# Performance work log

Hardware: AMD Instinct MI355X
Metric: run time of the kernel (lower is better)

The kernel has to match this reference:

```python
import jax, jax.numpy as jnp
import numpy as np
import math

# ---- static config (matches init_kwargs) ----
N_USERS = 40000
N_ITEMS = 30000
N_ENTITIES = 80000
N_REL = 8            # edge_type in [1, N_REL), relation_emb has N_REL-1 rows
DIM = 64
N_HEADS = 2
D_K = DIM // N_HEADS
N_HOPS = 2
E_KG = 800000
E_UI = 600000


def setup_inputs() -> dict:
    key = jax.random.key(0)
    ks = jax.random.split(key, 10)
    return {
        "user_emb": jax.random.normal(ks[0], (N_USERS, DIM), jnp.float32) * 0.1,
        "entity_emb": jax.random.normal(ks[1], (N_ENTITIES, DIM), jnp.float32) * 0.1,
        "relation_emb": jax.random.normal(ks[2], (N_REL - 1, DIM), jnp.float32) * 0.1,
        "W_Q": jax.random.normal(ks[3], (DIM, DIM), jnp.float32) * (1.0 / math.sqrt(DIM)),
        "inter_edge_w": jax.random.uniform(ks[4], (E_UI,), jnp.float32),
        "edge_head": jax.random.randint(ks[5], (E_KG,), 0, N_ENTITIES, jnp.int32),
        "edge_tail": jax.random.randint(ks[6], (E_KG,), 0, N_ENTITIES, jnp.int32),
        "edge_type": jax.random.randint(ks[7], (E_KG,), 1, N_REL, jnp.int32),
        "inter_user": jax.random.randint(ks[8], (E_UI,), 0, N_USERS, jnp.int32),
        "inter_item": jax.random.randint(ks[9], (E_UI,), 0, N_ENTITIES, jnp.int32),
    }


def _seg_softmax(x, seg, n):
    """Numerically-stable softmax over edges grouped by segment id (scatter_softmax)."""
    m = jax.ops.segment_max(x, seg, num_segments=n)
    m = jnp.where(jnp.isneginf(m), 0.0, m)          # empty segments
    ex = jnp.exp(x - m[seg])
    s = jax.ops.segment_sum(ex, seg, num_segments=n)
    return ex / (s[seg] + 1e-16)


def _edge_attn(entity_emb, relation_emb, W_Q, head, tail, etype):
    """Per-edge multi-head attention logits: q_h . (k_h * rel_h) / sqrt(d_k). [E, H]"""
    q = (entity_emb[head] @ W_Q).reshape(-1, N_HEADS, D_K)
    k = (entity_emb[tail] @ W_Q).reshape(-1, N_HEADS, D_K)
    k = k * relation_emb[etype - 1].reshape(-1, N_HEADS, D_K)
    return (q * k).sum(-1) * (1.0 / math.sqrt(D_K))


def _l2norm(x):
    return x / jnp.maximum(jnp.linalg.norm(x, axis=-1, keepdims=True), 1e-12)


def reference(user_emb, entity_emb, relation_emb, W_Q, inter_edge_w,
              edge_head, edge_tail, edge_type, inter_user, inter_item):
    # ---- norm_attn_computer (logits detached in original torch code) ----
    logits = jax.lax.stop_gradient(
        _edge_attn(entity_emb, relation_emb, W_Q, edge_head, edge_tail, edge_type).mean(-1))  # [E]
    score = _seg_softmax(logits, edge_head, N_ENTITIES)
    deg = jax.ops.segment_sum(jnp.ones((E_KG,), jnp.float32), edge_head, num_segments=N_ENTITIES)
    edge_attn_score = score * deg[edge_head]                                   # [E]
    item_attn_sumed = (jax.ops.segment_sum(logits, edge_head, num_segments=N_ENTITIES)
                       + jax.ops.segment_sum(logits, edge_tail, num_segments=N_ENTITIES))[:N_ITEMS]

    # ---- HGT message passing hops (mess_dropout=False) ----
    e, u = entity_emb, user_emb
    e_res, u_res = entity_emb, user_emb
    for _ in range(N_HOPS):
        attn = _edge_attn(e, relation_emb, W_Q, edge_head, edge_tail, edge_type)  # [E, H]
        s = _seg_softmax(attn, edge_head, N_ENTITIES)                              # [E, H]
        neigh = (e[edge_tail] * relation_emb[edge_type - 1]).reshape(-1, N_HEADS, D_K) * s[..., None]
        e_agg = jax.ops.segment_sum(neigh.reshape(-1, DIM), edge_head, num_segments=N_ENTITIES)
        # bipartite user<->item aggregation with interaction weights
        u_agg = jax.ops.segment_sum(inter_edge_w[:, None] * e[inter_item], inter_user,
                                    num_segments=N_USERS)
        e_agg = e_agg + jax.ops.segment_sum(inter_edge_w[:, None] * u[inter_user], inter_item,
                                            num_segments=N_ENTITIES)
        e, u = _l2norm(e_agg), _l2norm(u_agg)
        e_res, u_res = e_res + e, u_res + u

    node_res_emb = jnp.concatenate([u_res, e_res], axis=0)   # [N_USERS+N_ENTITIES, DIM]
    return node_res_emb, edge_attn_score, item_attn_sumed
```

## Files before the change

### kernel.cpp

```cpp
#include <hip/hip_runtime.h>
#include <math.h>

#define NUSERS 40000
#define NENT   80000
#define NITEMS 30000
#define DIM    64
#define EKG    800000
#define EUI    600000
#define NTOT   (NENT + NUSERS + NENT)
#define UBASE  NENT
#define IBASE  (NENT + NUSERS)

struct __align__(8) us4 { unsigned short x, y, z, w; };
static __device__ __forceinline__ float b2f(unsigned short b) {
    return __uint_as_float(((unsigned)b) << 16);
}
static __device__ __forceinline__ unsigned short f2b(float f) {
    unsigned u = __float_as_uint(f);
    return (unsigned short)((u + 0x7FFFu + ((u >> 16) & 1u)) >> 16);
}
static __device__ __forceinline__ float4 ld4b(const unsigned short* p) {
    us4 v = *(const us4*)p;
    return make_float4(b2f(v.x), b2f(v.y), b2f(v.z), b2f(v.w));
}
static __device__ __forceinline__ void st4b(unsigned short* p, float a, float b, float c, float d) {
    us4 v = {f2b(a), f2b(b), f2b(c), f2b(d)};
    *(us4*)p = v;
}

static __device__ __forceinline__ float grp16_sum(float v) {
    v += __shfl_xor(v, 1);
    v += __shfl_xor(v, 2);
    v += __shfl_xor(v, 4);
    v += __shfl_xor(v, 8);
    return v;
}

__global__ void count_kernel(const int* __restrict__ ehead, const int* __restrict__ etail,
                             const int* __restrict__ etype,
                             const int* __restrict__ iuser, const int* __restrict__ iitem,
                             int* __restrict__ cnt,
                             int* __restrict__ hrK, int* __restrict__ hrU, int* __restrict__ hrI,
                             int* __restrict__ tpack) {
    int e = blockIdx.x * blockDim.x + threadIdx.x;
    if (e < EKG) {
        int h = __builtin_nontemporal_load(&ehead[e]);
        int r = atomicAdd(&cnt[h], 1);
        hrK[e] = (h << 15) | r;
        tpack[e] = __builtin_nontemporal_load(&etail[e]) |
                   ((__builtin_nontemporal_load(&etype[e]) - 1) << 20);
    }
    if (e < EUI) {
        int u = __builtin_nontemporal_load(&iuser[e]);
        int r = atomicAdd(&cnt[UBASE + u], 1);
        hrU[e] = (u << 16) | r;
        int it = __builtin_nontemporal_load(&iitem[e]);
        int r2 = atomicAdd(&cnt[IBASE + it], 1);
        hrI[e] = (it << 15) | r2;
    }
}

#define SCHUNK 2048
#define SBLOCKS ((NTOT + SCHUNK - 1) / SCHUNK)

__global__ void scanA_kernel(const int* __restrict__ cnt, int* __restrict__ bsum) {
    int b = blockIdx.x, tid = threadIdx.x;
    int base = b * SCHUNK + tid * 8;
    int ts = 0;
#pragma unroll
    for (int k = 0; k < 8; k++) {
        int i = base + k;
        ts += (i < NTOT) ? cnt[i] : 0;
    }
#pragma unroll
    for (int d = 1; d < 64; d <<= 1) ts += __shfl_xor(ts, d);
    __shared__ int ws[4];
    if ((tid & 63) == 0) ws[tid >> 6] = ts;
    __syncthreads();
    if (tid == 0) bsum[b] = ws[0] + ws[1] + ws[2] + ws[3];
}

__global__ void scanB_kernel(const int* __restrict__ bsum, int* __restrict__ bpre,
                             int* __restrict__ off) {
    int lane = threadIdx.x;
    int carry = 0;
    for (int base = 0; base < SBLOCKS; base += 64) {
        int i = base + lane;
        int x = (i < SBLOCKS) ? bsum[i] : 0;
        int inc = x;
#pragma unroll
        for (int d = 1; d < 64; d <<= 1) {
            int t = __shfl_up(inc, d);
            if (lane >= d) inc += t;
        }
        if (i < SBLOCKS) bpre[i] = carry + inc - x;
        carry += __shfl(inc, 63);
    }
    if (lane == 0) off[NTOT] = carry;
}

__global__ void scanC_kernel(const int* __restrict__ cnt, const int* __restrict__ bpre,
                             int* __restrict__ off) {
    __shared__ int wtot[4];
    int b = blockIdx.x, tid = threadIdx.x, lane = tid & 63, wid = tid >> 6;
    int base = b * SCHUNK + tid * 8;
    int vals[8];
    int ts = 0;
#pragma unroll
    for (int k = 0; k < 8; k++) {
        int i = base + k;
        int x = (i < NTOT) ? cnt[i] : 0;
        vals[k] = ts;
        ts += x;
    }
    int inc = ts;
#pragma unroll
    for (int d = 1; d < 64; d <<= 1) {
        int t = __shfl_up(inc, d);
        if (lane >= d) inc += t;
    }
    if (lane == 63) wtot[wid] = inc;
    __syncthreads();
    int wbase = 0;
    for (int w = 0; w < wid; w++) wbase += wtot[w];
    int tbase = bpre[b] + wbase + (inc - ts);
#pragma unroll
    for (int k = 0; k < 8; k++) {
        int i = base + k;
        if (i < NTOT) off[i] = tbase + vals[k];
    }
}

__global__ void fillKG_kernel(const int* __restrict__ hrK, const int* __restrict__ tpack,
                              const int* __restrict__ off,
                              int* __restrict__ tt, int* __restrict__ eid, int lo, int hi) {
    int e = blockIdx.x * blockDim.x + threadIdx.x;
    if (e >= EKG) return;
    int v = __builtin_nontemporal_load(&hrK[e]);
    int h = ((unsigned)v) >> 15;
    if (h < (unsigned)lo || h >= (unsigned)hi) return;
    int p = off[h] + (v & 0x7FFF);
    tt[p] = __builtin_nontemporal_load(&tpack[e]);
    eid[p] = e;
}

__global__ void fillUIu_kernel(const int* __restrict__ hrU, const int* __restrict__ iitem,
                               const float* __restrict__ iwin, const int* __restrict__ off,
                               int2* __restrict__ upack, int lo, int hi) {
    int e = blockIdx.x * blockDim.x + threadIdx.x;
    if (e >= EUI) return;
    int v = __builtin_nontemporal_load(&hrU[e]);
    int u = ((unsigned)v) >> 16;
    if (u < (unsigned)lo || u >= (unsigned)hi) return;
    int p = off[UBASE + u] - EKG + (v & 0xFFFF);
    upack[p] = make_int2(__builtin_nontemporal_load(&iitem[e]),
                         __float_as_int(__builtin_nontemporal_load(&iwin[e])));
}

__global__ void fillUIi_kernel(const int* __restrict__ hrI, const int* __restrict__ iuser,
                               const float* __restrict__ iwin, const int* __restrict__ off,
                               int2* __restrict__ ipack, int lo, int hi) {
    int e = blockIdx.x * blockDim.x + threadIdx.x;
    if (e >= EUI) return;
    int v = __builtin_nontemporal_load(&hrI[e]);
    int it = ((unsigned)v) >> 15;
    if (it < (unsigned)lo || it >= (unsigned)hi) return;
    int p = off[IBASE + it] - (EKG + EUI) + (v & 0x7FFF);
    ipack[p] = make_int2(__builtin_nontemporal_load(&iuser[e]),
                         __float_as_int(__builtin_nontemporal_load(&iwin[e])));
}

__global__ void cvt_kernel(const float* __restrict__ in, unsigned short* __restrict__ out,
                           int n4) {
    int i = blockIdx.x * blockDim.x + threadIdx.x;
    if (i >= n4) return;
    float4 v = *(const float4*)(in + (size_t)i * 4);
    st4b(out + (size_t)i * 4, v.x, v.y, v.z, v.w);
}

template <int MODE>
__global__ void gemm_wq_kernel(const float* __restrict__ Xf,
                               const unsigned short* __restrict__ Xb_in,
                               const float* __restrict__ W,
                               unsigned short* __restrict__ Pb,
                               unsigned short* __restrict__ Xb_out) {
    __shared__ float Wl[64 * 64];
    int tid = threadIdx.x;
    for (int i = tid; i < 64 * 64; i += 256) Wl[i] = W[i];
    __syncthreads();
    int rloc = tid >> 4;
    int c4 = (tid & 15) * 4;
    int row = blockIdx.x * 16 + rloc;
    float ax = 0, ay = 0, az = 0, aw = 0;
#pragma unroll 8
    for (int d = 0; d < 64; d++) {
        float xv = (MODE == 0) ? Xf[(size_t)row * DIM + d] : b2f(Xb_in[(size_t)row * DIM + d]);
        const float4 w = *(const float4*)&Wl[d * 64 + c4];
        ax += xv * w.x;
        ay += xv * w.y;
        az += xv * w.z;
        aw += xv * w.w;
    }
    st4b(Pb + (size_t)row * DIM + c4, ax, ay, az, aw);
    if (MODE == 0) {
        const float4 xx = *(const float4*)(Xf + (size_t)row * DIM + c4);
        st4b(Xb_out + (size_t)row * DIM + c4, xx.x, xx.y, xx.z, xx.w);
    }
}

template <bool HOP0>
__global__ void hop_kernel(const unsigned short* __restrict__ Pb,
                           const unsigned short* __restrict__ eb,
                           const unsigned short* __restrict__ ub,
                           const float* __restrict__ rel,
                           const int* __restrict__ off,
                           const int* __restrict__ tt, const int* __restrict__ eid,
                           const int2* __restrict__ upack, const int2* __restrict__ ipack,
                           const float* __restrict__ ebase, const float* __restrict__ ubase,
                           const unsigned short* __restrict__ eprevb,
                           const unsigned short* __restrict__ uprevb,
                           float* __restrict__ e_res, float* __restrict__ u_res,
                           unsigned short* __restrict__ enxtb, unsigned short* __restrict__ unxtb,
                           float* __restrict__ logit, float* __restrict__ edge_score,
                           float* __restrict__ item_sum) {
    __shared__ float srel[7 * DIM];
    int tid = threadIdx.x;
    for (int i = tid; i < 7 * DIM; i += 256) srel[i] = rel[i];
    __syncthreads();
    int g = tid >> 4, l = tid & 15;
    int v = blockIdx.x * 16 + g;
    const float sc = 0.17677669529663687f;
    float ax = 0, ay = 0, az = 0, aw = 0;

    if (v < NENT) {
        int o0 = off[v], o1 = off[v + 1];
        int deg = o1 - o0;
        const float4 q = ld4b(Pb + (size_t)v * DIM + l * 4);
        float s_h = 0.f;
        float s_lm = 0.f, lsum = 0.f;
        for (int j = o0; j < o1; j++) {
            unsigned t = (unsigned)tt[j];
            int tail = t & 0xFFFFF;
            int r = t >> 20;
            const float4 k = ld4b(Pb + (size_t)tail * DIM + l * 4);
            const float4 ev = ld4b(eb + (size_t)tail * DIM + l * 4);
            const float4 rv = *(const float4*)(srel + r * DIM + l * 4);
            float part = q.x * k.x * rv.x + q.y * k.y * rv.y + q.z * k.z * rv.z + q.w * k.w * rv.w;
            part += __shfl_xor(part, 1);
            part += __shfl_xor(part, 2);
            part += __shfl_xor(part, 4);
            part *= sc;
            float w = __expf(part);
            s_h += w;
            ax += w * ev.x * rv.x;
            ay += w * ev.y * rv.y;
            az += w * ev.z * rv.z;
            aw += w * ev.w * rv.w;
            if (HOP0) {
                float other = __shfl_xor(part, 8);
                float lm = 0.5f * (part + other);
                s_lm += __expf(lm);
                lsum += lm;
                if (l == 0) {
                    logit[j] = lm;
                    if (tail < NITEMS) atomicAdd(&item_sum[tail], lm);
                }
            }
        }
        float inv_sh = 1.0f / (s_h + 1e-16f);
        ax *= inv_sh;
        ay *= inv_sh;
        az *= inv_sh;
        aw *= inv_sh;
        if (HOP0) {
            if (l == 0 && v < NITEMS && deg > 0) atomicAdd(&item_sum[v], lsum);
            float inv_slm = 1.0f / (s_lm + 1e-16f);
            float degf = (float)deg;
            for (int j = o0 + l; j < o1; j += 16) {
                edge_score[eid[j]] = __expf(logit[j]) * inv_slm * degf;
            }
        }
        int p0 = off[IBASE + v] - (EKG + EUI);
        int p1 = off[IBASE + v + 1] - (EKG + EUI);
        for (int j = p0; j < p1; j++) {
            int2 up = ipack[j];
            float w = __int_as_float(up.y);
            const float4 uv = ld4b(ub + (size_t)up.x * DIM + l * 4);
            ax += w * uv.x;
            ay += w * uv.y;
            az += w * uv.z;
            aw += w * uv.w;
        }
        float nsq = grp16_sum(ax * ax + ay * ay + az * az + aw * aw);
        float invn = 1.0f / fmaxf(sqrtf(nsq), 1e-12f);
        float ox = ax * invn, oy = ay * invn, oz = az * invn, ow = aw * invn;
        size_t base = (size_t)v * DIM + l * 4;
        if (HOP0) {
            st4b(enxtb + base, ox, oy, oz, ow);
        } else {
            const float4 b0 = *(const float4*)(ebase + base);
            const float4 p0v = ld4b(eprevb + base);
            float4 ro = {b0.x + p0v.x + ox, b0.y + p0v.y + oy, b0.z + p0v.z + oz,
                         b0.w + p0v.w + ow};
            *(float4*)(e_res + base) = ro;
        }
    } else {
        int u = v - NENT;
        int p0 = off[UBASE + u] - EKG;
        int p1 = off[UBASE + u + 1] - EKG;
        for (int j = p0; j < p1; j++) {
            int2 up = upack[j];
            float w = __int_as_float(up.y);
            const float4 ev = ld4b(eb + (size_t)up.x * DIM + l * 4);
            ax += w * ev.x;
            ay += w * ev.y;
            az += w * ev.z;
            aw += w * ev.w;
        }
        float nsq = grp16_sum(ax * ax + ay * ay + az * az + aw * aw);
        float invn = 1.0f / fmaxf(sqrtf(nsq), 1e-12f);
        float ox = ax * invn, oy = ay * invn, oz = az * invn, ow = aw * invn;
        size_t base = (size_t)u * DIM + l * 4;
        if (HOP0) {
            st4b(unxtb + base, ox, oy, oz, ow);
        } else {
            const float4 b0 = *(const float4*)(ubase + base);
            const float4 p0v = ld4b(uprevb + base);
            float4 ro = {b0.x + p0v.x + ox, b0.y + p0v.y + oy, b0.z + p0v.z + oz,
                         b0.w + p0v.w + ow};
            *(float4*)(u_res + base) = ro;
        }
    }
}

extern "C" void kernel_launch(void* const* d_in, const int* in_sizes, int n_in,
                              void* d_out, int out_size, void* d_ws, size_t ws_size,
                              hipStream_t stream) {
    const float* user_emb   = (const float*)d_in[0];
    const float* entity_emb = (const float*)d_in[1];
    const float* rel        = (const float*)d_in[2];
    const float* W_Q        = (const float*)d_in[3];
    const float* iwin       = (const float*)d_in[4];
    const int* ehead        = (const int*)d_in[5];
    const int* etail        = (const int*)d_in[6];
    const int* etype        = (const int*)d_in[7];
    const int* iuser        = (const int*)d_in[8];
    const int* iitem        = (const int*)d_in[9];

    float* out        = (float*)d_out;
    float* u_res      = out;
    float* e_res      = out + (size_t)NUSERS * DIM;
    float* edge_score = out + (size_t)(NUSERS + NENT) * DIM;
    float* item_sum   = edge_score + EKG;

    char* w = (char*)d_ws;
    auto alloc = [&](size_t bytes) -> void* {
        void* p = (void*)w;
        w += (bytes + 255) & ~(size_t)255;
        return p;
    };
    unsigned short* Pb  = (unsigned short*)alloc((size_t)NENT * DIM * 2);
    unsigned short* e0b = (unsigned short*)alloc((size_t)NENT * DIM * 2);
    unsigned short* eAb = (unsigned short*)alloc((size_t)NENT * DIM * 2);
    unsigned short* u0b = (unsigned short*)alloc((size_t)NUSERS * DIM * 2);
    unsigned short* uAb = (unsigned short*)alloc((size_t)NUSERS * DIM * 2);
    int* tt      = (int*)alloc((size_t)EKG * 4);
    int* eid     = (int*)alloc((size_t)EKG * 4);
    int2* upack  = (int2*)alloc((size_t)EUI * 8);
    int2* ipack  = (int2*)alloc((size_t)EUI * 8);
    int* hrK     = (int*)alloc((size_t)EKG * 4);
    int* hrU     = (int*)alloc((size_t)EUI * 4);
    int* hrI     = (int*)alloc((size_t)EUI * 4);
    int* tpack   = (int*)alloc((size_t)EKG * 4);
    float* logit = (float*)alloc((size_t)EKG * 4);
    int* cnt     = (int*)alloc((size_t)NTOT * 4);
    int* off     = (int*)alloc((size_t)(NTOT + 1) * 4);
    int* bsum    = (int*)alloc((size_t)SBLOCKS * 4);
    int* bpre    = (int*)alloc((size_t)SBLOCKS * 4);
    (void)ws_size; (void)in_sizes; (void)n_in; (void)out_size;

    hipMemsetAsync(cnt, 0, (size_t)NTOT * 4, stream);
    hipMemsetAsync(item_sum, 0, (size_t)NITEMS * 4, stream);

    count_kernel<<<(EKG + 255) / 256, 256, 0, stream>>>(ehead, etail, etype, iuser, iitem, cnt,
                                                        hrK, hrU, hrI, tpack);
    scanA_kernel<<<SBLOCKS, 256, 0, stream>>>(cnt, bsum);
    scanB_kernel<<<1, 64, 0, stream>>>(bsum, bpre, off);
    scanC_kernel<<<SBLOCKS, 256, 0, stream>>>(cnt, bpre, off);

    const int KGG = (EKG + 255) / 256, UIG = (EUI + 255) / 256;
    for (int p = 0; p < 2; p++)
        fillKG_kernel<<<KGG, 256, 0, stream>>>(hrK, tpack, off, tt, eid,
                                               p * 40000, (p + 1) * 40000);
    for (int p = 0; p < 2; p++)
        fillUIu_kernel<<<UIG, 256, 0, stream>>>(hrU, iitem, iwin, off, upack,
                                                p * 20000, (p + 1) * 20000);
    for (int p = 0; p < 2; p++)
        fillUIi_kernel<<<UIG, 256, 0, stream>>>(hrI, iuser, iwin, off, ipack,
                                                p * 40000, (p + 1) * 40000);

    cvt_kernel<<<(NUSERS * DIM / 4 + 255) / 256, 256, 0, stream>>>(user_emb, u0b,
                                                                   NUSERS * DIM / 4);

    const int HOPG = (NENT + NUSERS) / 16;

    gemm_wq_kernel<0><<<NENT / 16, 256, 0, stream>>>(entity_emb, nullptr, W_Q, Pb, e0b);
    hop_kernel<true><<<HOPG, 256, 0, stream>>>(Pb, e0b, u0b, rel, off, tt, eid, upack, ipack,
                                               nullptr, nullptr, nullptr, nullptr, nullptr,
                                               nullptr, eAb, uAb, logit, edge_score, item_sum);

    gemm_wq_kernel<1><<<NENT / 16, 256, 0, stream>>>(nullptr, eAb, W_Q, Pb, nullptr);
    hop_kernel<false><<<HOPG, 256, 0, stream>>>(Pb, eAb, uAb, rel, off, tt, eid, upack, ipack,
                                                entity_emb, user_emb, eAb, uAb, e_res, u_res,
                                                nullptr, nullptr, nullptr, nullptr, nullptr);
}
```

Baseline: 385.8 us.

## Interleave projected and raw entity rows, pack KG edge arrays, fold small kernels

Entity projections and bf16 embeddings are stored interleaved in one 128-wide row per entity, so each gathered tail fetches both vectors from the same 256-byte region. Tail and edge-id arrays are packed into one int2 array. The gather loops are unrolled by two to keep more loads in flight. The user conversion moves into count_kernel and the item_sum memset into the first GEMM, which removes a launch and a memset. The hop-0 output is written into the second table's embedding half, and the GEMM there reads its input from that half.

```diff
diff --git a/kernel.cpp b/kernel.cpp
--- a/kernel.cpp
+++ b/kernel.cpp
@@ -19,9 +19,11 @@
     unsigned u = __float_as_uint(f);
     return (unsigned short)((u + 0x7FFFu + ((u >> 16) & 1u)) >> 16);
 }
+static __device__ __forceinline__ float4 us4tof(us4 v) {
+    return make_float4(b2f(v.x), b2f(v.y), b2f(v.z), b2f(v.w));
+}
 static __device__ __forceinline__ float4 ld4b(const unsigned short* p) {
-    us4 v = *(const us4*)p;
-    return make_float4(b2f(v.x), b2f(v.y), b2f(v.z), b2f(v.w));
+    return us4tof(*(const us4*)p);
 }
 static __device__ __forceinline__ void st4b(unsigned short* p, float a, float b, float c, float d) {
     us4 v = {f2b(a), f2b(b), f2b(c), f2b(d)};
@@ -39,9 +41,10 @@
 __global__ void count_kernel(const int* __restrict__ ehead, const int* __restrict__ etail,
                              const int* __restrict__ etype,
                              const int* __restrict__ iuser, const int* __restrict__ iitem,
+                             const float* __restrict__ user_emb,
                              int* __restrict__ cnt,
                              int* __restrict__ hrK, int* __restrict__ hrU, int* __restrict__ hrI,
-                             int* __restrict__ tpack) {
+                             int* __restrict__ tpack, unsigned short* __restrict__ u0b) {
     int e = blockIdx.x * blockDim.x + threadIdx.x;
     if (e < EKG) {
         int h = __builtin_nontemporal_load(&ehead[e]);
@@ -57,6 +60,10 @@
         int it = __builtin_nontemporal_load(&iitem[e]);
         int r2 = atomicAdd(&cnt[IBASE + it], 1);
         hrI[e] = (it << 15) | r2;
+    }
+    if (e < NUSERS * (DIM / 4)) {
+        float4 vv = *(const float4*)(user_emb + (size_t)e * 4);
+        st4b(u0b + (size_t)e * 4, vv.x, vv.y, vv.z, vv.w);
     }
 }
 
@@ -133,15 +140,14 @@
 
 __global__ void fillKG_kernel(const int* __restrict__ hrK, const int* __restrict__ tpack,
                               const int* __restrict__ off,
-                              int* __restrict__ tt, int* __restrict__ eid, int lo, int hi) {
+                              int2* __restrict__ kgp, int lo, int hi) {
     int e = blockIdx.x * blockDim.x + threadIdx.x;
     if (e >= EKG) return;
     int v = __builtin_nontemporal_load(&hrK[e]);
     int h = ((unsigned)v) >> 15;
     if (h < (unsigned)lo || h >= (unsigned)hi) return;
     int p = off[h] + (v & 0x7FFF);
-    tt[p] = __builtin_nontemporal_load(&tpack[e]);
-    eid[p] = e;
+    kgp[p] = make_int2(__builtin_nontemporal_load(&tpack[e]), e);
 }
 
 __global__ void fillUIu_kernel(const int* __restrict__ hrU, const int* __restrict__ iitem,
@@ -170,20 +176,11 @@
                          __float_as_int(__builtin_nontemporal_load(&iwin[e])));
 }
 
-__global__ void cvt_kernel(const float* __restrict__ in, unsigned short* __restrict__ out,
-                           int n4) {
-    int i = blockIdx.x * blockDim.x + threadIdx.x;
-    if (i >= n4) return;
-    float4 v = *(const float4*)(in + (size_t)i * 4);
-    st4b(out + (size_t)i * 4, v.x, v.y, v.z, v.w);
-}
-
 template <int MODE>
 __global__ void gemm_wq_kernel(const float* __restrict__ Xf,
-                               const unsigned short* __restrict__ Xb_in,
+                               unsigned short* __restrict__ T,
                                const float* __restrict__ W,
-                               unsigned short* __restrict__ Pb,
-                               unsigned short* __restrict__ Xb_out) {
+                               float* __restrict__ item_sum) {
     __shared__ float Wl[64 * 64];
     int tid = threadIdx.x;
     for (int i = tid; i < 64 * 64; i += 256) Wl[i] = W[i];
@@ -194,33 +191,32 @@
     float ax = 0, ay = 0, az = 0, aw = 0;
 #pragma unroll 8
     for (int d = 0; d < 64; d++) {
-        float xv = (MODE == 0) ? Xf[(size_t)row * DIM + d] : b2f(Xb_in[(size_t)row * DIM + d]);
+        float xv = (MODE == 0) ? Xf[(size_t)row * DIM + d] : b2f(T[(size_t)row * 128 + 64 + d]);
         const float4 w = *(const float4*)&Wl[d * 64 + c4];
         ax += xv * w.x;
         ay += xv * w.y;
         az += xv * w.z;
         aw += xv * w.w;
     }
-    st4b(Pb + (size_t)row * DIM + c4, ax, ay, az, aw);
+    st4b(T + (size_t)row * 128 + c4, ax, ay, az, aw);
     if (MODE == 0) {
         const float4 xx = *(const float4*)(Xf + (size_t)row * DIM + c4);
-        st4b(Xb_out + (size_t)row * DIM + c4, xx.x, xx.y, xx.z, xx.w);
+        st4b(T + (size_t)row * 128 + 64 + c4, xx.x, xx.y, xx.z, xx.w);
+        int gid = blockIdx.x * 256 + tid;
+        if (gid < NITEMS) item_sum[gid] = 0.f;
     }
 }
 
 template <bool HOP0>
-__global__ void hop_kernel(const unsigned short* __restrict__ Pb,
-                           const unsigned short* __restrict__ eb,
+__global__ void hop_kernel(const unsigned short* __restrict__ T,
                            const unsigned short* __restrict__ ub,
                            const float* __restrict__ rel,
                            const int* __restrict__ off,
-                           const int* __restrict__ tt, const int* __restrict__ eid,
+                           const int2* __restrict__ kgp,
                            const int2* __restrict__ upack, const int2* __restrict__ ipack,
                            const float* __restrict__ ebase, const float* __restrict__ ubase,
-                           const unsigned short* __restrict__ eprevb,
-                           const unsigned short* __restrict__ uprevb,
                            float* __restrict__ e_res, float* __restrict__ u_res,
-                           unsigned short* __restrict__ enxtb, unsigned short* __restrict__ unxtb,
+                           unsigned short* __restrict__ Tnxt, unsigned short* __restrict__ unxt,
                            float* __restrict__ logit, float* __restrict__ edge_score,
                            float* __restrict__ item_sum) {
     __shared__ float srel[7 * DIM];
@@ -235,37 +231,52 @@
     if (v < NENT) {
         int o0 = off[v], o1 = off[v + 1];
         int deg = o1 - o0;
-        const float4 q = ld4b(Pb + (size_t)v * DIM + l * 4);
-        float s_h = 0.f;
-        float s_lm = 0.f, lsum = 0.f;
-        for (int j = o0; j < o1; j++) {
-            unsigned t = (unsigned)tt[j];
-            int tail = t & 0xFFFFF;
+        const float4 q = ld4b(T + (size_t)v * 128 + l * 4);
+        float s_h = 0.f, s_lm = 0.f, lsum = 0.f;
+
+        auto edge_compute = [&](unsigned t, int jj, float4 k, float4 ev) {
             int r = t >> 20;
-            const float4 k = ld4b(Pb + (size_t)tail * DIM + l * 4);
-            const float4 ev = ld4b(eb + (size_t)tail * DIM + l * 4);
             const float4 rv = *(const float4*)(srel + r * DIM + l * 4);
             float part = q.x * k.x * rv.x + q.y * k.y * rv.y + q.z * k.z * rv.z + q.w * k.w * rv.w;
             part += __shfl_xor(part, 1);
             part += __shfl_xor(part, 2);
             part += __shfl_xor(part, 4);
             part *= sc;
-            float w = __expf(part);
-            s_h += w;
-            ax += w * ev.x * rv.x;
-            ay += w * ev.y * rv.y;
-            az += w * ev.z * rv.z;
-            aw += w * ev.w * rv.w;
+            float wgt = __expf(part);
+            s_h += wgt;
+            ax += wgt * ev.x * rv.x;
+            ay += wgt * ev.y * rv.y;
+            az += wgt * ev.z * rv.z;
+            aw += wgt * ev.w * rv.w;
             if (HOP0) {
                 float other = __shfl_xor(part, 8);
                 float lm = 0.5f * (part + other);
                 s_lm += __expf(lm);
                 lsum += lm;
                 if (l == 0) {
-                    logit[j] = lm;
+                    logit[jj] = lm;
+                    int tail = t & 0xFFFFF;
                     if (tail < NITEMS) atomicAdd(&item_sum[tail], lm);
                 }
             }
+        };
+
+        int j = o0;
+        for (; j + 2 <= o1; j += 2) {
+            int2 kp0 = kgp[j], kp1 = kgp[j + 1];
+            const unsigned short* b0 = T + (size_t)((unsigned)kp0.x & 0xFFFFF) * 128 + l * 4;
+            const unsigned short* b1 = T + (size_t)((unsigned)kp1.x & 0xFFFFF) * 128 + l * 4;
+            us4 rk0 = *(const us4*)b0;
+            us4 re0 = *(const us4*)(b0 + 64);
+            us4 rk1 = *(const us4*)b1;
+            us4 re1 = *(const us4*)(b1 + 64);
+            edge_compute((unsigned)kp0.x, j, us4tof(rk0), us4tof(re0));
+            edge_compute((unsigned)kp1.x, j + 1, us4tof(rk1), us4tof(re1));
+        }
+        if (j < o1) {
+            int2 kp0 = kgp[j];
+            const unsigned short* b0 = T + (size_t)((unsigned)kp0.x & 0xFFFFF) * 128 + l * 4;
+            edge_compute((unsigned)kp0.x, j, ld4b(b0), ld4b(b0 + 64));
         }
         float inv_sh = 1.0f / (s_h + 1e-16f);
         ax *= inv_sh;
@@ -273,61 +284,84 @@
         az *= inv_sh;
         aw *= inv_sh;
         if (HOP0) {
-            if (l == 0 && v < NITEMS && deg > 0) atomicAdd(&item_sum[v], lsum);
+            if (l == 0 && deg > 0 && v < NITEMS) atomicAdd(&item_sum[v], lsum);
             float inv_slm = 1.0f / (s_lm + 1e-16f);
             float degf = (float)deg;
-            for (int j = o0 + l; j < o1; j += 16) {
-                edge_score[eid[j]] = __expf(logit[j]) * inv_slm * degf;
-            }
+            for (int jj = o0 + l; jj < o1; jj += 16)
+                edge_score[kgp[jj].y] = __expf(logit[jj]) * inv_slm * degf;
         }
         int p0 = off[IBASE + v] - (EKG + EUI);
         int p1 = off[IBASE + v + 1] - (EKG + EUI);
-        for (int j = p0; j < p1; j++) {
-            int2 up = ipack[j];
-            float w = __int_as_float(up.y);
-            const float4 uv = ld4b(ub + (size_t)up.x * DIM + l * 4);
-            ax += w * uv.x;
-            ay += w * uv.y;
-            az += w * uv.z;
-            aw += w * uv.w;
+        int j2 = p0;
+        for (; j2 + 2 <= p1; j2 += 2) {
+            int2 a = ipack[j2], b = ipack[j2 + 1];
+            us4 ra = *(const us4*)(ub + (size_t)a.x * 64 + l * 4);
+            us4 rb = *(const us4*)(ub + (size_t)b.x * 64 + l * 4);
+            float wa = __int_as_float(a.y), wb = __int_as_float(b.y);
+            float4 fa = us4tof(ra), fb = us4tof(rb);
+            ax += wa * fa.x + wb * fb.x;
+            ay += wa * fa.y + wb * fb.y;
+            az += wa * fa.z + wb * fb.z;
+            aw += wa * fa.w + wb * fb.w;
+        }
+        if (j2 < p1) {
+            int2 a = ipack[j2];
+            float wa = __int_as_float(a.y);
+            float4 fa = ld4b(ub + (size_t)a.x * 64 + l * 4);
+            ax += wa * fa.x;
+            ay += wa * fa.y;
+            az += wa * fa.z;
+            aw += wa * fa.w;
         }
         float nsq = grp16_sum(ax * ax + ay * ay + az * az + aw * aw);
         float invn = 1.0f / fmaxf(sqrtf(nsq), 1e-12f);
         float ox = ax * invn, oy = ay * invn, oz = az * invn, ow = aw * invn;
-        size_t base = (size_t)v * DIM + l * 4;
         if (HOP0) {
-            st4b(enxtb + base, ox, oy, oz, ow);
+            st4b(Tnxt + (size_t)v * 128 + 64 + l * 4, ox, oy, oz, ow);
         } else {
-            const float4 b0 = *(const float4*)(ebase + base);
-            const float4 p0v = ld4b(eprevb + base);
-            float4 ro = {b0.x + p0v.x + ox, b0.y + p0v.y + oy, b0.z + p0v.z + oz,
-                         b0.w + p0v.w + ow};
+            size_t base = (size_t)v * DIM + l * 4;
+            const float4 b0v = *(const float4*)(ebase + base);
+            const float4 pv = ld4b(T + (size_t)v * 128 + 64 + l * 4);
+            float4 ro = {b0v.x + pv.x + ox, b0v.y + pv.y + oy, b0v.z + pv.z + oz,
+                         b0v.w + pv.w + ow};
             *(float4*)(e_res + base) = ro;
         }
     } else {
         int u = v - NENT;
         int p0 = off[UBASE + u] - EKG;
         int p1 = off[UBASE + u + 1] - EKG;
-        for (int j = p0; j < p1; j++) {
-            int2 up = upack[j];
-            float w = __int_as_float(up.y);
-            const float4 ev = ld4b(eb + (size_t)up.x * DIM + l * 4);
-            ax += w * ev.x;
-            ay += w * ev.y;
-            az += w * ev.z;
-            aw += w * ev.w;
+        int j2 = p0;
+        for (; j2 + 2 <= p1; j2 += 2) {
+            int2 a = upack[j2], b = upack[j2 + 1];
+            us4 ra = *(const us4*)(T + (size_t)a.x * 128 + 64 + l * 4);
+            us4 rb = *(const us4*)(T + (size_t)b.x * 128 + 64 + l * 4);
+            float wa = __int_as_float(a.y), wb = __int_as_float(b.y);
+            float4 fa = us4tof(ra), fb = us4tof(rb);
+            ax += wa * fa.x + wb * fb.x;
+            ay += wa * fa.y + wb * fb.y;
+            az += wa * fa.z + wb * fb.z;
+            aw += wa * fa.w + wb * fb.w;
+        }
+        if (j2 < p1) {
+            int2 a = upack[j2];
+            float wa = __int_as_float(a.y);
+            float4 fa = ld4b(T + (size_t)a.x * 128 + 64 + l * 4);
+            ax += wa * fa.x;
+            ay += wa * fa.y;
+            az += wa * fa.z;
+            aw += wa * fa.w;
         }
         float nsq = grp16_sum(ax * ax + ay * ay + az * az + aw * aw);
         float invn = 1.0f / fmaxf(sqrtf(nsq), 1e-12f);
         float ox = ax * invn, oy = ay * invn, oz = az * invn, ow = aw * invn;
-        size_t base = (size_t)u * DIM + l * 4;
         if (HOP0) {
-            st4b(unxtb + base, ox, oy, oz, ow);
+            st4b(unxt + (size_t)u * DIM + l * 4, ox, oy, oz, ow);
         } else {
-            const float4 b0 = *(const float4*)(ubase + base);
-            const float4 p0v = ld4b(uprevb + base);
-            float4 ro = {b0.x + p0v.x + ox, b0.y + p0v.y + oy, b0.z + p0v.z + oz,
-                         b0.w + p0v.w + ow};
+            size_t base = (size_t)u * DIM + l * 4;
+            const float4 b0v = *(const float4*)(ubase + base);
+            const float4 pv = ld4b(ub + base);
+            float4 ro = {b0v.x + pv.x + ox, b0v.y + pv.y + oy, b0v.z + pv.z + oz,
+                         b0v.w + pv.w + ow};
             *(float4*)(u_res + base) = ro;
         }
     }
@@ -359,13 +393,11 @@
         w += (bytes + 255) & ~(size_t)255;
         return p;
     };
-    unsigned short* Pb  = (unsigned short*)alloc((size_t)NENT * DIM * 2);
-    unsigned short* e0b = (unsigned short*)alloc((size_t)NENT * DIM * 2);
-    unsigned short* eAb = (unsigned short*)alloc((size_t)NENT * DIM * 2);
+    unsigned short* T0  = (unsigned short*)alloc((size_t)NENT * 128 * 2);
+    unsigned short* T1  = (unsigned short*)alloc((size_t)NENT * 128 * 2);
     unsigned short* u0b = (unsigned short*)alloc((size_t)NUSERS * DIM * 2);
     unsigned short* uAb = (unsigned short*)alloc((size_t)NUSERS * DIM * 2);
-    int* tt      = (int*)alloc((size_t)EKG * 4);
-    int* eid     = (int*)alloc((size_t)EKG * 4);
+    int2* kgp    = (int2*)alloc((size_t)EKG * 8);
     int2* upack  = (int2*)alloc((size_t)EUI * 8);
     int2* ipack  = (int2*)alloc((size_t)EUI * 8);
     int* hrK     = (int*)alloc((size_t)EKG * 4);
@@ -380,17 +412,16 @@
     (void)ws_size; (void)in_sizes; (void)n_in; (void)out_size;
 
     hipMemsetAsync(cnt, 0, (size_t)NTOT * 4, stream);
-    hipMemsetAsync(item_sum, 0, (size_t)NITEMS * 4, stream);
-
-    count_kernel<<<(EKG + 255) / 256, 256, 0, stream>>>(ehead, etail, etype, iuser, iitem, cnt,
-                                                        hrK, hrU, hrI, tpack);
+
+    count_kernel<<<(EKG + 255) / 256, 256, 0, stream>>>(ehead, etail, etype, iuser, iitem,
+                                                        user_emb, cnt, hrK, hrU, hrI, tpack, u0b);
     scanA_kernel<<<SBLOCKS, 256, 0, stream>>>(cnt, bsum);
     scanB_kernel<<<1, 64, 0, stream>>>(bsum, bpre, off);
     scanC_kernel<<<SBLOCKS, 256, 0, stream>>>(cnt, bpre, off);
 
     const int KGG = (EKG + 255) / 256, UIG = (EUI + 255) / 256;
     for (int p = 0; p < 2; p++)
-        fillKG_kernel<<<KGG, 256, 0, stream>>>(hrK, tpack, off, tt, eid,
+        fillKG_kernel<<<KGG, 256, 0, stream>>>(hrK, tpack, off, kgp,
                                                p * 40000, (p + 1) * 40000);
     for (int p = 0; p < 2; p++)
         fillUIu_kernel<<<UIG, 256, 0, stream>>>(hrU, iitem, iwin, off, upack,
@@ -399,18 +430,15 @@
         fillUIi_kernel<<<UIG, 256, 0, stream>>>(hrI, iuser, iwin, off, ipack,
                                                 p * 40000, (p + 1) * 40000);
 
-    cvt_kernel<<<(NUSERS * DIM / 4 + 255) / 256, 256, 0, stream>>>(user_emb, u0b,
-                                                                   NUSERS * DIM / 4);
-
     const int HOPG = (NENT + NUSERS) / 16;
 
-    gemm_wq_kernel<0><<<NENT / 16, 256, 0, stream>>>(entity_emb, nullptr, W_Q, Pb, e0b);
-    hop_kernel<true><<<HOPG, 256, 0, stream>>>(Pb, e0b, u0b, rel, off, tt, eid, upack, ipack,
-                                               nullptr, nullptr, nullptr, nullptr, nullptr,
-                                               nullptr, eAb, uAb, logit, edge_score, item_sum);
-
-    gemm_wq_kernel<1><<<NENT / 16, 256, 0, stream>>>(nullptr, eAb, W_Q, Pb, nullptr);
-    hop_kernel<false><<<HOPG, 256, 0, stream>>>(Pb, eAb, uAb, rel, off, tt, eid, upack, ipack,
-                                                entity_emb, user_emb, eAb, uAb, e_res, u_res,
+    gemm_wq_kernel<0><<<NENT / 16, 256, 0, stream>>>(entity_emb, T0, W_Q, item_sum);
+    hop_kernel<true><<<HOPG, 256, 0, stream>>>(T0, u0b, rel, off, kgp, upack, ipack,
+                                               nullptr, nullptr, nullptr, nullptr,
+                                               T1, uAb, logit, edge_score, item_sum);
+
+    gemm_wq_kernel<1><<<NENT / 16, 256, 0, stream>>>(nullptr, T1, W_Q, nullptr);
+    hop_kernel<false><<<HOPG, 256, 0, stream>>>(T1, uAb, rel, off, kgp, upack, ipack,
+                                                entity_emb, user_emb, e_res, u_res,
                                                 nullptr, nullptr, nullptr, nullptr, nullptr);
 }
```

Measured after the change: 326.7 us. 15.3% less time.
